# Kernel tuning notes

Hardware: AMD Instinct MI355X
Metric: run time of the kernel (lower is better)

The kernel has to match this reference:

```python
import jax, jax.numpy as jnp
import numpy as np

E = 8            # moe_num_experts
HIDDEN = 1024    # hidden_size
FFN = 4096       # ffn_hidden_size
TOKENS = 8192    # total tokens, pre-sorted by expert; balanced -> TOKENS // E per expert


def setup_inputs() -> dict:
    key = jax.random.key(0)
    k1, k2, k3 = jax.random.split(key, 3)
    x = jax.random.normal(k1, (TOKENS, HIDDEN), dtype=jnp.float32)
    # w1, w2 stored flattened as [E*FFN, HIDDEN], matching create_dmoe_expert_weights' view([-1, columns])
    w1 = jax.random.normal(k2, (E * FFN, HIDDEN), dtype=jnp.float32) * (1.0 / np.sqrt(HIDDEN))
    w2 = jax.random.normal(k3, (E * FFN, HIDDEN), dtype=jnp.float32) * (1.0 / np.sqrt(FFN))
    return {"x": x, "w1": w1, "w2": w2, "num_experts": E}


def reference(x, w1, w2, num_experts):
    # Block-diagonal topology of dMoE SparseMLP: tokens sorted by expert, each
    # expert owns a contiguous FFN slice of w1/w2. Equivalent grouped GEMM:
    #   out_e = gelu(x_e @ w1_e^T) @ w2_e   (megablocks gelu = tanh-approx GELU)
    tokens, hidden = x.shape
    ffn = w1.shape[0] // num_experts
    tpe = tokens // num_experts  # tokens per expert (balanced topology)
    xe = x.reshape(num_experts, tpe, hidden)        # [E, T/E, H]
    w1e = w1.reshape(num_experts, ffn, hidden)      # [E, F, H]
    w2e = w2.reshape(num_experts, ffn, hidden)      # [E, F, H]
    h = jax.nn.gelu(jnp.einsum('eth,efh->etf', xe, w1e), approximate=True)  # sdd + gelu
    out = jnp.einsum('etf,efh->eth', h, w2e)        # dsd
    return out.reshape(tokens, hidden)
```

## Files before the change

### kernel.cpp

```cpp
#include <hip/hip_runtime.h>
#include <hip/hip_bf16.h>
#include <stdint.h>

#define NE 8
#define HID 1024
#define FFN 4096
#define TOK 8192
#define TPE (TOK / NE)

typedef __attribute__((ext_vector_type(8))) short    bf16x8;
typedef __attribute__((ext_vector_type(4))) float    f32x4;
typedef __attribute__((ext_vector_type(4))) unsigned short ushort4v;
typedef __attribute__((ext_vector_type(8))) unsigned short ushort8v;


__device__ __forceinline__ unsigned short f2bf(float f) {
    union { float f; unsigned u; } c; c.f = f;
    unsigned r = c.u + 0x7fffu + ((c.u >> 16) & 1u);
    return (unsigned short)(r >> 16);
}

__device__ __forceinline__ float gelu_tanh(float x) {
    const float c0 = 0.7978845608028654f;
    const float c1 = 0.044715f;
    float u = c0 * (x + c1 * x * x * x);
    float t = 1.0f - 2.0f / (1.0f + __expf(2.0f * u));
    return 0.5f * x * (1.0f + t);
}

typedef const __attribute__((address_space(1))) void gbl_void_t;
typedef __attribute__((address_space(3))) void lds_void_t;

__device__ __forceinline__ void gload_lds16(const void* g, void* l) {
    __builtin_amdgcn_global_load_lds((gbl_void_t*)g, (lds_void_t*)l, 16, 0, 0);
}


__global__ void transpose_cvt(const float* __restrict__ in,
                              unsigned short* __restrict__ out) {
    __shared__ unsigned short tile[64][65];
    const int e  = blockIdx.z;
    const int f0 = blockIdx.x * 64;
    const int h0 = blockIdx.y * 64;
    const float*     src = in  + (size_t)e * FFN * HID;
    unsigned short*  dst = out + (size_t)e * HID * FFN;
    const int t  = threadIdx.x;
    const int tr = t >> 4;
    const int tc = (t & 15) * 4;
#pragma unroll
    for (int i = 0; i < 4; i++) {
        int f = i * 16 + tr;
        f32x4 v = *(const f32x4*)(src + (size_t)(f0 + f) * HID + h0 + tc);
#pragma unroll
        for (int j = 0; j < 4; j++) tile[f][tc + j] = f2bf(v[j]);
    }
    __syncthreads();
#pragma unroll
    for (int i = 0; i < 4; i++) {
        int h = i * 16 + tr;
        ushort4v o;
#pragma unroll
        for (int j = 0; j < 4; j++) o[j] = tile[tc + j][h];
        *(ushort4v*)(dst + (size_t)(h0 + h) * FFN + f0 + tc) = o;
    }
}


template <int GX, int GY>
__global__ __launch_bounds__(512, 2)
void gemm8f(const float* __restrict__ Af,
            const float* __restrict__ Bf,
            unsigned short* __restrict__ Cout, int M, int N, int K) {
    constexpr int BM = 256, BN = 256, BK = 64;
    constexpr int NH = 2, NI = 4, S = 32;
    constexpr int ABYTES = BM * BK * 2;
    constexpr int BBYTES = BN * BK * 2;
    constexpr int BUF = ABYTES + BBYTES;
    constexpr int NWG = NE * GX * GY;

    __shared__ __align__(16) char lds[2 * BUF];

    const int lin = blockIdx.x;
    const int wid = (lin & 7) * (NWG >> 3) + (lin >> 3);
    const int e   = wid / (GX * GY);
    const int rem = wid % (GX * GY);
    const int m0  = (rem % GX) * BM;
    const int n0  = (rem / GX) * BN;

    const float* Ae = Af + (size_t)e * M * K;
    const float* Be = Bf + (size_t)e * N * K;

    const int tid  = threadIdx.x;
    const int lane = tid & 63;
    const int w    = tid >> 6;
    const int wr   = w >> 2, wc = w & 3;
    const int fr   = lane & 15, fq = lane >> 4;

    const int rA  = tid >> 3;
    const int kb  = (tid & 7) * 16;
    const int kbs = kb ^ ((rA & 7) << 4);
    const int eoff = kbs >> 1;
    const float* aFb = Ae + (size_t)(m0 + rA) * K + eoff;
    const int   fB   = (rA / S) * 2 * S + (rA % S);
    const float* bFb = Be + (size_t)(n0 + fB) * K + eoff;
    char* dA0 = lds + rA * 128 + kb;
    char* dA1 = dA0 + BUF;
    char* dB0 = lds + ABYTES + fB * 128 + kb;
    char* dB1 = dB0 + BUF;

    auto LD_A = [&](int au, int kt, f32x4 (&g)[4]) {
        const float* s = aFb + (size_t)kt * 64;
        g[0] = *(const f32x4*)(s + (size_t)(au * 64) * K);
        g[1] = *(const f32x4*)(s + (size_t)(au * 64) * K + 4);
        g[2] = *(const f32x4*)(s + (size_t)(au * 64 + 128) * K);
        g[3] = *(const f32x4*)(s + (size_t)(au * 64 + 128) * K + 4);
    };
    auto LD_B = [&](int bu, int kt, f32x4 (&g)[4]) {
        const float* s = bFb + (size_t)kt * 64;
        g[0] = *(const f32x4*)(s + (size_t)(bu * S) * K);
        g[1] = *(const f32x4*)(s + (size_t)(bu * S) * K + 4);
        g[2] = *(const f32x4*)(s + (size_t)(bu * S + 128) * K);
        g[3] = *(const f32x4*)(s + (size_t)(bu * S + 128) * K + 4);
    };
    auto PACK = [&](const f32x4& lo, const f32x4& hi) {
        ushort8v o;
#pragma unroll
        for (int j = 0; j < 4; j++) { o[j] = f2bf(lo[j]); o[4 + j] = f2bf(hi[j]); }
        return o;
    };
    auto WR_A = [&](int au, char* d, f32x4 (&g)[4]) {
        *(ushort8v*)(d + (au * 64) * 128)       = PACK(g[0], g[1]);
        *(ushort8v*)(d + (au * 64 + 128) * 128) = PACK(g[2], g[3]);
    };
    auto WR_B = [&](int bu, char* d, f32x4 (&g)[4]) {
        *(ushort8v*)(d + (bu * S) * 128)        = PACK(g[0], g[1]);
        *(ushort8v*)(d + (bu * S + 128) * 128)  = PACK(g[2], g[3]);
    };

    const int kx0 = (fq * 16) ^ ((lane & 7) << 4);
    const char* paA = lds + (wr * 128 + fr) * 128;
    const char* paB = lds + ABYTES + (wc * (BN / 4) + fr) * 128;
    const char* pa0k0 = paA + kx0;        const char* pa0k1 = paA + (kx0 ^ 64);
    const char* pa1k0 = pa0k0 + BUF;      const char* pa1k1 = pa0k1 + BUF;
    const char* pb0k0 = paB + kx0;        const char* pb0k1 = paB + (kx0 ^ 64);
    const char* pb1k0 = pb0k0 + BUF;      const char* pb1k1 = pb0k1 + BUF;

    bf16x8 a[4][2], b0[NH][2], b1[NH][2];

    auto LDA = [&](const char* p0, const char* p1, int mq) {
#pragma unroll
        for (int mi = 0; mi < 4; mi++) {
            a[mi][0] = *(const bf16x8*)(p0 + mq * 8192 + mi * 2048);
            a[mi][1] = *(const bf16x8*)(p1 + mq * 8192 + mi * 2048);
        }
    };
    auto LDB = [&](const char* p0, const char* p1, int nq, bf16x8 (&bb)[NH][2]) {
#pragma unroll
        for (int ni = 0; ni < NH; ni++) {
            bb[ni][0] = *(const bf16x8*)(p0 + (nq * (BN / 8) + ni * 16) * 128);
            bb[ni][1] = *(const bf16x8*)(p1 + (nq * (BN / 8) + ni * 16) * 128);
        }
    };

    f32x4 acc[8][NI];

    auto MMQ = [&](int mq, int nq, bf16x8 (&bb)[NH][2]) {
        __builtin_amdgcn_s_setprio(1);
#pragma unroll
        for (int mi = 0; mi < 4; mi++)
#pragma unroll
            for (int ni = 0; ni < NH; ni++) {
                f32x4& c = acc[mq * 4 + mi][nq * NH + ni];
                c = __builtin_amdgcn_mfma_f32_16x16x32_bf16(a[mi][0], bb[ni][0], c, 0, 0, 0);
                c = __builtin_amdgcn_mfma_f32_16x16x32_bf16(a[mi][1], bb[ni][1], c, 0, 0, 0);
            }
        __builtin_amdgcn_s_setprio(0);
    };

#define MIDBAR()  __builtin_amdgcn_s_barrier();                                      \
                  asm volatile("s_waitcnt lgkmcnt(0)" ::: "memory")
#define ENDBAR()  __builtin_amdgcn_s_barrier()
#define LGHINT()  asm volatile("s_waitcnt lgkmcnt(8)" ::: "memory")

    const int NT   = K / BK;
    const int NTm1 = NT - 1;

    f32x4 gO[4], gE[4];
    {
        f32x4 t0[4];
        LD_A(0, 0, t0); WR_A(0, dA0, t0);
        LD_A(1, 0, t0); WR_A(1, dA0, t0);
        LD_B(0, 0, t0); WR_B(0, dB0, t0);
        LD_B(1, 0, t0); WR_B(1, dB0, t0);
        LD_A(0, 1, t0); WR_A(0, dA1, t0);
        LD_B(0, 1, t0); WR_B(0, dB1, t0);
        LD_B(1, 1, t0); WR_B(1, dB1, t0);
    }
    LD_A(1, 1, gO);
    LD_A(0, (2 < NT ? 2 : NTm1), gE);
#pragma unroll
    for (int i = 0; i < 8; i++)
#pragma unroll
        for (int j = 0; j < NI; j++) acc[i][j] = f32x4{0.f, 0.f, 0.f, 0.f};
    asm volatile("s_waitcnt lgkmcnt(0)" ::: "memory");
    __builtin_amdgcn_s_barrier();

    const int NW = NT / 2;
    for (int ww = 0; ww < NW; ++ww) {
        const int T = 2 * ww;
        const int kt2 = (T + 2 < NT) ? T + 2 : NTm1;
        const int kt3 = (T + 3 < NT) ? T + 3 : NTm1;
        const int kt4 = (T + 4 < NT) ? T + 4 : NTm1;

        LDA(pa0k0, pa0k1, 0); LDB(pb0k0, pb0k1, 0, b0); LGHINT();
        MIDBAR();
        WR_A(1, dA1, gO); LD_B(0, kt2, gO);
        MMQ(0, 0, b0); ENDBAR();
        LDB(pb0k0, pb0k1, 1, b1);
        MIDBAR();
        WR_A(0, dA0, gE); LD_B(1, kt2, gE);
        MMQ(0, 1, b1); ENDBAR();
        LDA(pa0k0, pa0k1, 1);
        MIDBAR();
        WR_B(0, dB0, gO); LD_A(1, kt2, gO);
        MMQ(1, 1, b1); ENDBAR();
        MIDBAR();
        WR_B(1, dB0, gE); LD_A(0, kt3, gE);
        MMQ(1, 0, b0); ENDBAR();
        LDA(pa1k0, pa1k1, 0); LDB(pb1k0, pb1k1, 0, b0); LGHINT();
        MIDBAR();
        WR_A(1, dA0, gO); LD_B(0, kt3, gO);
        MMQ(0, 0, b0); ENDBAR();
        LDB(pb1k0, pb1k1, 1, b1);
        MIDBAR();
        WR_A(0, dA1, gE); LD_B(1, kt3, gE);
        MMQ(0, 1, b1); ENDBAR();
        LDA(pa1k0, pa1k1, 1);
        MIDBAR();
        WR_B(0, dB1, gO); LD_A(1, kt3, gO);
        MMQ(1, 1, b1); ENDBAR();
        MIDBAR();
        WR_B(1, dB1, gE); LD_A(0, kt4, gE);
        MMQ(1, 0, b0); ENDBAR();
    }

    const int r0 = m0 + wr * 128 + fq * 4;
    const int c0 = n0 + wc * (BN / 4) + fr;
    unsigned short* C = Cout + (size_t)e * M * N;
#pragma unroll
    for (int mi = 0; mi < 8; mi++)
#pragma unroll
        for (int ni = 0; ni < NI; ni++) {
            int row = r0 + mi * 16, col = c0 + ni * 16;
#pragma unroll
            for (int r = 0; r < 4; r++)
                C[(size_t)(row + r) * N + col] = f2bf(gelu_tanh(acc[mi][ni][r]));
        }
#undef MIDBAR
#undef ENDBAR
#undef LGHINT
}


template <int BN, int GX, int GY, bool GELU>
__global__ __launch_bounds__(512, 2)
void gemm8p(const unsigned short* __restrict__ A,
            const unsigned short* __restrict__ B,
            void* __restrict__ Cout, int M, int N, int K) {
    constexpr int BM = 256, BK = 64;
    constexpr int NH = BN / 128;
    constexpr int NI = 2 * NH;
    constexpr int LB = BN / 128;
    constexpr int S  = BN / 8;
    constexpr int ABYTES = BM * BK * 2;
    constexpr int BBYTES = BN * BK * 2;
    constexpr int BUF = ABYTES + BBYTES;
    constexpr int VMC = 2 + 2 * LB;
    constexpr int NWG = NE * GX * GY;

    __shared__ __align__(16) char lds[2 * BUF];

    const int lin = blockIdx.x;
    const int wid = (lin & 7) * (NWG >> 3) + (lin >> 3);
    const int e   = wid / (GX * GY);
    const int rem = wid % (GX * GY);
    const int m0  = (rem % GX) * BM;
    const int n0  = (rem / GX) * BN;

    const size_t K2 = (size_t)K * 2;
    const char* Ae = (const char*)(A + (size_t)e * M * K);
    const char* Be = (const char*)(B + (size_t)e * N * K);

    const int tid  = threadIdx.x;
    const int lane = tid & 63;
    const int w    = tid >> 6;
    const int wr   = w >> 2, wc = w & 3;
    const int fr   = lane & 15, fq = lane >> 4;

    const int rA  = tid >> 3;
    const int kb  = (tid & 7) * 16;
    const int kbs = kb ^ ((rA & 7) << 4);
    const char* aptr = Ae + (size_t)(m0 + rA) * K2 + kbs;
    const int   fB   = (rA / S) * 2 * S + (rA % S);
    const char* bptr = Be + (size_t)(n0 + fB) * K2 + kbs;
    char* dA0 = lds + rA * 128 + kb;
    char* dA1 = dA0 + BUF;
    char* dB0 = lds + ABYTES + fB * 128 + kb;
    char* dB1 = dB0 + BUF;

    auto SA = [&](int au, int kt, char* d) {
        const char* s = aptr + (size_t)kt * 128;
#pragma unroll
        for (int i = 0; i < 2; i++)
            gload_lds16(s + (size_t)(au * 64 + i * 128) * K2,
                        d + (au * 64 + i * 128) * 128);
    };
    auto SB = [&](int bu, int kt, char* d) {
        const char* s = bptr + (size_t)kt * 128;
#pragma unroll
        for (int i = 0; i < LB; i++)
            gload_lds16(s + (size_t)(bu * S + i * 128) * K2,
                        d + (bu * S + i * 128) * 128);
    };

    const int kx0 = (fq * 16) ^ ((lane & 7) << 4);
    const char* paA = lds + (wr * 128 + fr) * 128;
    const char* paB = lds + ABYTES + (wc * (BN / 4) + fr) * 128;
    const char* pa0k0 = paA + kx0;        const char* pa0k1 = paA + (kx0 ^ 64);
    const char* pa1k0 = pa0k0 + BUF;      const char* pa1k1 = pa0k1 + BUF;
    const char* pb0k0 = paB + kx0;        const char* pb0k1 = paB + (kx0 ^ 64);
    const char* pb1k0 = pb0k0 + BUF;      const char* pb1k1 = pb0k1 + BUF;

    f32x4 acc[8][NI];
#pragma unroll
    for (int i = 0; i < 8; i++)
#pragma unroll
        for (int j = 0; j < NI; j++) acc[i][j] = f32x4{0.f, 0.f, 0.f, 0.f};

    bf16x8 a[4][2], b0[NH][2], b1[NH][2];

    auto LDA = [&](const char* p0, const char* p1, int mq) {
#pragma unroll
        for (int mi = 0; mi < 4; mi++) {
            a[mi][0] = *(const bf16x8*)(p0 + mq * 8192 + mi * 2048);
            a[mi][1] = *(const bf16x8*)(p1 + mq * 8192 + mi * 2048);
        }
    };
    auto LDB = [&](const char* p0, const char* p1, int nq, bf16x8 (&bb)[NH][2]) {
#pragma unroll
        for (int ni = 0; ni < NH; ni++) {
            bb[ni][0] = *(const bf16x8*)(p0 + (nq * (BN / 8) + ni * 16) * 128);
            bb[ni][1] = *(const bf16x8*)(p1 + (nq * (BN / 8) + ni * 16) * 128);
        }
    };
    auto MMQ = [&](int mq, int nq, bf16x8 (&bb)[NH][2]) {
        __builtin_amdgcn_s_setprio(1);
#pragma unroll
        for (int mi = 0; mi < 4; mi++)
#pragma unroll
            for (int ni = 0; ni < NH; ni++) {
                f32x4& c = acc[mq * 4 + mi][nq * NH + ni];
                c = __builtin_amdgcn_mfma_f32_16x16x32_bf16(a[mi][0], bb[ni][0], c, 0, 0, 0);
                c = __builtin_amdgcn_mfma_f32_16x16x32_bf16(a[mi][1], bb[ni][1], c, 0, 0, 0);
            }
        __builtin_amdgcn_s_setprio(0);
    };

#define MIDBAR()  __builtin_amdgcn_s_barrier();                                      \
                  asm volatile("s_waitcnt lgkmcnt(0)" ::: "memory")
#define ENDBAR()  __builtin_amdgcn_s_barrier()
#define LGHINT()  asm volatile("s_waitcnt lgkmcnt(8)" ::: "memory")
#define VMW()     asm volatile("s_waitcnt vmcnt(%0)" :: "n"(VMC) : "memory")

    const int NT   = K / BK;
    const int NTm1 = NT - 1;

    SA(0, 0, dA0); SB(0, 0, dB0); SB(1, 0, dB0); SA(1, 0, dA0);
    SA(0, 1, dA1); SB(0, 1, dB1); SB(1, 1, dB1);
    VMW();
    __builtin_amdgcn_s_barrier();

    const int NW = NT / 2;
    for (int ww = 0; ww < NW; ++ww) {
        const int T = 2 * ww;
        const int kt1 = T + 1;
        const int kt2 = (T + 2 < NT) ? T + 2 : NTm1;
        const int kt3 = (T + 3 < NT) ? T + 3 : NTm1;

        LDA(pa0k0, pa0k1, 0); LDB(pb0k0, pb0k1, 0, b0); SA(1, kt1, dA1); LGHINT();
        MIDBAR(); MMQ(0, 0, b0); ENDBAR();
        LDB(pb0k0, pb0k1, 1, b1); SA(0, kt2, dA0);
        MIDBAR(); MMQ(0, 1, b1); ENDBAR();
        LDA(pa0k0, pa0k1, 1); SB(0, kt2, dB0);
        MIDBAR(); MMQ(1, 1, b1); ENDBAR();
        SB(1, kt2, dB0);
        MIDBAR(); MMQ(1, 0, b0); VMW(); ENDBAR();
        LDA(pa1k0, pa1k1, 0); LDB(pb1k0, pb1k1, 0, b0); SA(1, kt2, dA0); LGHINT();
        MIDBAR(); MMQ(0, 0, b0); ENDBAR();
        LDB(pb1k0, pb1k1, 1, b1); SA(0, kt3, dA1);
        MIDBAR(); MMQ(0, 1, b1); ENDBAR();
        LDA(pa1k0, pa1k1, 1); SB(0, kt3, dB1);
        MIDBAR(); MMQ(1, 1, b1); ENDBAR();
        SB(1, kt3, dB1);
        MIDBAR(); MMQ(1, 0, b0); VMW(); ENDBAR();
    }
    asm volatile("s_waitcnt vmcnt(0)" ::: "memory");

    const int r0 = m0 + wr * 128 + fq * 4;
    const int c0 = n0 + wc * (BN / 4) + fr;
    if constexpr (GELU) {
        unsigned short* C = (unsigned short*)Cout + (size_t)e * M * N;
#pragma unroll
        for (int mi = 0; mi < 8; mi++)
#pragma unroll
            for (int ni = 0; ni < NI; ni++) {
                int row = r0 + mi * 16, col = c0 + ni * 16;
#pragma unroll
                for (int r = 0; r < 4; r++)
                    C[(size_t)(row + r) * N + col] = f2bf(gelu_tanh(acc[mi][ni][r]));
            }
    } else {
        float* C = (float*)Cout + (size_t)e * M * N;
#pragma unroll
        for (int mi = 0; mi < 8; mi++)
#pragma unroll
            for (int ni = 0; ni < NI; ni++) {
                int row = r0 + mi * 16, col = c0 + ni * 16;
#pragma unroll
                for (int r = 0; r < 4; r++)
                    C[(size_t)(row + r) * N + col] = acc[mi][ni][r];
            }
    }
#undef MIDBAR
#undef ENDBAR
#undef LGHINT
#undef VMW
}


__global__ void fused_fallback(const float* __restrict__ x,
                               const float* __restrict__ w1,
                               const float* __restrict__ w2,
                               float* __restrict__ out) {
    __shared__ float xs[HID];
    __shared__ float hs[FFN];
    const int tok = blockIdx.x;
    const int e   = tok / TPE;
    const float* w1e = w1 + (size_t)e * FFN * HID;
    const float* w2e = w2 + (size_t)e * FFN * HID;
    const int t = threadIdx.x;
    for (int i = t; i < HID; i += 256) xs[i] = x[(size_t)tok * HID + i];
    __syncthreads();
    for (int f = t; f < FFN; f += 256) {
        const float* wr_ = w1e + (size_t)f * HID;
        float s = 0.f;
        for (int k = 0; k < HID; k++) s += xs[k] * wr_[k];
        hs[f] = gelu_tanh(s);
    }
    __syncthreads();
    for (int h = t; h < HID; h += 256) {
        float s = 0.f;
        for (int f = 0; f < FFN; f++) s += hs[f] * w2e[(size_t)f * HID + h];
        out[(size_t)tok * HID + h] = s;
    }
}


extern "C" void kernel_launch(void* const* d_in, const int* in_sizes, int n_in,
                              void* d_out, int out_size, void* d_ws, size_t ws_size,
                              hipStream_t stream) {
    const float* x  = (const float*)d_in[0];
    const float* w1 = (const float*)d_in[1];
    const float* w2 = (const float*)d_in[2];
    float* out = (float*)d_out;

    const size_t W2B = (size_t)NE * FFN * HID * 2;
    const size_t HB  = (size_t)TOK * FFN * 2;
    const size_t need = W2B + HB;

    if (ws_size >= need) {
        char* ws = (char*)d_ws;
        unsigned short* w2t = (unsigned short*)ws;
        unsigned short* hb  = (unsigned short*)(ws + W2B);

        transpose_cvt<<<dim3(FFN / 64, HID / 64, NE), 256, 0, stream>>>(w2, w2t);

        gemm8f<TPE / 256, FFN / 256><<<NE * (TPE / 256) * (FFN / 256), 512, 0, stream>>>(
            x, w1, hb, TPE, FFN, HID);
        gemm8p<128, TPE / 256, HID / 128, false><<<NE * (TPE / 256) * (HID / 128), 512, 0, stream>>>(
            hb, w2t, out, TPE, HID, FFN);
    } else {
        fused_fallback<<<TOK, 256, 0, stream>>>(x, w1, w2, out);
    }
}
```

Before: 233.0 us.

## Remap second GEMM waves to a 4x2 grid with 64x64 per-wave tiles

The second grouped GEMM (h @ w2) drops its generic BN template and uses a fixed 256x128 block tile. The 8 waves are now arranged 4x2 instead of 2x4, so each wave computes a 64x64 sub-tile (interleaved rows and columns) rather than 128x32. This changes per-wave LDS read volume and register accumulator count, and is meant to improve operand reuse and reduce register pressure. The lgkmcnt hint wait is removed, which leaves the LDS load scheduling to the barriers.

Result: no change. 229.8 us (-1.4%).

```diff
diff --git a/kernel.cpp b/kernel.cpp
--- a/kernel.cpp
+++ b/kernel.cpp
@@ -262,20 +262,17 @@
 }
 
 
-template <int BN, int GX, int GY, bool GELU>
+template <int GX, int GY>
 __global__ __launch_bounds__(512, 2)
-void gemm8p(const unsigned short* __restrict__ A,
+void gemm2q(const unsigned short* __restrict__ A,
             const unsigned short* __restrict__ B,
-            void* __restrict__ Cout, int M, int N, int K) {
-    constexpr int BM = 256, BK = 64;
-    constexpr int NH = BN / 128;
-    constexpr int NI = 2 * NH;
-    constexpr int LB = BN / 128;
+            float* __restrict__ Cout, int M, int N, int K) {
+    constexpr int BM = 256, BN = 128, BK = 64;
     constexpr int S  = BN / 8;
     constexpr int ABYTES = BM * BK * 2;
     constexpr int BBYTES = BN * BK * 2;
     constexpr int BUF = ABYTES + BBYTES;
-    constexpr int VMC = 2 + 2 * LB;
+    constexpr int VMC = 4;
     constexpr int NWG = NE * GX * GY;
 
     __shared__ __align__(16) char lds[2 * BUF];
@@ -294,7 +291,8 @@
     const int tid  = threadIdx.x;
     const int lane = tid & 63;
     const int w    = tid >> 6;
-    const int wr   = w >> 2, wc = w & 3;
+    const int wr   = w >> 1;
+    const int wc   = w & 1;
     const int fr   = lane & 15, fq = lane >> 4;
 
     const int rA  = tid >> 3;
@@ -317,49 +315,48 @@
     };
     auto SB = [&](int bu, int kt, char* d) {
         const char* s = bptr + (size_t)kt * 128;
-#pragma unroll
-        for (int i = 0; i < LB; i++)
-            gload_lds16(s + (size_t)(bu * S + i * 128) * K2,
-                        d + (bu * S + i * 128) * 128);
-    };
-
-    const int kx0 = (fq * 16) ^ ((lane & 7) << 4);
-    const char* paA = lds + (wr * 128 + fr) * 128;
-    const char* paB = lds + ABYTES + (wc * (BN / 4) + fr) * 128;
+        gload_lds16(s + (size_t)(bu * S) * K2, d + (bu * S) * 128);
+    };
+
+    const int kx0   = (fq * 16) ^ ((lane & 7) << 4);
+    const int aBase = (wr & 1) * 32 + (wr >> 1) * 128;
+    const int bBase = wc * 64;
+    const char* paA = lds + (aBase + fr) * 128;
+    const char* paB = lds + ABYTES + (bBase + fr) * 128;
     const char* pa0k0 = paA + kx0;        const char* pa0k1 = paA + (kx0 ^ 64);
     const char* pa1k0 = pa0k0 + BUF;      const char* pa1k1 = pa0k1 + BUF;
     const char* pb0k0 = paB + kx0;        const char* pb0k1 = paB + (kx0 ^ 64);
     const char* pb1k0 = pb0k0 + BUF;      const char* pb1k1 = pb0k1 + BUF;
 
-    f32x4 acc[8][NI];
-#pragma unroll
-    for (int i = 0; i < 8; i++)
-#pragma unroll
-        for (int j = 0; j < NI; j++) acc[i][j] = f32x4{0.f, 0.f, 0.f, 0.f};
-
-    bf16x8 a[4][2], b0[NH][2], b1[NH][2];
+    f32x4 acc[4][4];
+#pragma unroll
+    for (int i = 0; i < 4; i++)
+#pragma unroll
+        for (int j = 0; j < 4; j++) acc[i][j] = f32x4{0.f, 0.f, 0.f, 0.f};
+
+    bf16x8 a[2][2], b0[2][2], b1[2][2];
 
     auto LDA = [&](const char* p0, const char* p1, int mq) {
 #pragma unroll
-        for (int mi = 0; mi < 4; mi++) {
+        for (int mi = 0; mi < 2; mi++) {
             a[mi][0] = *(const bf16x8*)(p0 + mq * 8192 + mi * 2048);
             a[mi][1] = *(const bf16x8*)(p1 + mq * 8192 + mi * 2048);
         }
     };
-    auto LDB = [&](const char* p0, const char* p1, int nq, bf16x8 (&bb)[NH][2]) {
-#pragma unroll
-        for (int ni = 0; ni < NH; ni++) {
-            bb[ni][0] = *(const bf16x8*)(p0 + (nq * (BN / 8) + ni * 16) * 128);
-            bb[ni][1] = *(const bf16x8*)(p1 + (nq * (BN / 8) + ni * 16) * 128);
-        }
-    };
-    auto MMQ = [&](int mq, int nq, bf16x8 (&bb)[NH][2]) {
+    auto LDB = [&](const char* p0, const char* p1, int nq, bf16x8 (&bb)[2][2]) {
+#pragma unroll
+        for (int ni = 0; ni < 2; ni++) {
+            bb[ni][0] = *(const bf16x8*)(p0 + (nq * 16 + ni * 32) * 128);
+            bb[ni][1] = *(const bf16x8*)(p1 + (nq * 16 + ni * 32) * 128);
+        }
+    };
+    auto MMQ = [&](int mq, int nq, bf16x8 (&bb)[2][2]) {
         __builtin_amdgcn_s_setprio(1);
 #pragma unroll
-        for (int mi = 0; mi < 4; mi++)
-#pragma unroll
-            for (int ni = 0; ni < NH; ni++) {
-                f32x4& c = acc[mq * 4 + mi][nq * NH + ni];
+        for (int mi = 0; mi < 2; mi++)
+#pragma unroll
+            for (int ni = 0; ni < 2; ni++) {
+                f32x4& c = acc[mq * 2 + mi][nq * 2 + ni];
                 c = __builtin_amdgcn_mfma_f32_16x16x32_bf16(a[mi][0], bb[ni][0], c, 0, 0, 0);
                 c = __builtin_amdgcn_mfma_f32_16x16x32_bf16(a[mi][1], bb[ni][1], c, 0, 0, 0);
             }
@@ -369,7 +366,6 @@
 #define MIDBAR()  __builtin_amdgcn_s_barrier();                                      \
                   asm volatile("s_waitcnt lgkmcnt(0)" ::: "memory")
 #define ENDBAR()  __builtin_amdgcn_s_barrier()
-#define LGHINT()  asm volatile("s_waitcnt lgkmcnt(8)" ::: "memory")
 #define VMW()     asm volatile("s_waitcnt vmcnt(%0)" :: "n"(VMC) : "memory")
 
     const int NT   = K / BK;
@@ -387,7 +383,7 @@
         const int kt2 = (T + 2 < NT) ? T + 2 : NTm1;
         const int kt3 = (T + 3 < NT) ? T + 3 : NTm1;
 
-        LDA(pa0k0, pa0k1, 0); LDB(pb0k0, pb0k1, 0, b0); SA(1, kt1, dA1); LGHINT();
+        LDA(pa0k0, pa0k1, 0); LDB(pb0k0, pb0k1, 0, b0); SA(1, kt1, dA1);
         MIDBAR(); MMQ(0, 0, b0); ENDBAR();
         LDB(pb0k0, pb0k1, 1, b1); SA(0, kt2, dA0);
         MIDBAR(); MMQ(0, 1, b1); ENDBAR();
@@ -395,7 +391,7 @@
         MIDBAR(); MMQ(1, 1, b1); ENDBAR();
         SB(1, kt2, dB0);
         MIDBAR(); MMQ(1, 0, b0); VMW(); ENDBAR();
-        LDA(pa1k0, pa1k1, 0); LDB(pb1k0, pb1k1, 0, b0); SA(1, kt2, dA0); LGHINT();
+        LDA(pa1k0, pa1k1, 0); LDB(pb1k0, pb1k1, 0, b0); SA(1, kt2, dA0);
         MIDBAR(); MMQ(0, 0, b0); ENDBAR();
         LDB(pb1k0, pb1k1, 1, b1); SA(0, kt3, dA1);
         MIDBAR(); MMQ(0, 1, b1); ENDBAR();
@@ -406,34 +402,21 @@
     }
     asm volatile("s_waitcnt vmcnt(0)" ::: "memory");
 
-    const int r0 = m0 + wr * 128 + fq * 4;
-    const int c0 = n0 + wc * (BN / 4) + fr;
-    if constexpr (GELU) {
-        unsigned short* C = (unsigned short*)Cout + (size_t)e * M * N;
-#pragma unroll
-        for (int mi = 0; mi < 8; mi++)
-#pragma unroll
-            for (int ni = 0; ni < NI; ni++) {
-                int row = r0 + mi * 16, col = c0 + ni * 16;
-#pragma unroll
-                for (int r = 0; r < 4; r++)
-                    C[(size_t)(row + r) * N + col] = f2bf(gelu_tanh(acc[mi][ni][r]));
-            }
-    } else {
-        float* C = (float*)Cout + (size_t)e * M * N;
-#pragma unroll
-        for (int mi = 0; mi < 8; mi++)
-#pragma unroll
-            for (int ni = 0; ni < NI; ni++) {
-                int row = r0 + mi * 16, col = c0 + ni * 16;
-#pragma unroll
-                for (int r = 0; r < 4; r++)
-                    C[(size_t)(row + r) * N + col] = acc[mi][ni][r];
-            }
-    }
+    const int r0 = m0 + aBase + fq * 4;
+    const int c0 = n0 + bBase + fr;
+    float* C = Cout + (size_t)e * M * N;
+#pragma unroll
+    for (int ai = 0; ai < 4; ai++)
+#pragma unroll
+        for (int aj = 0; aj < 4; aj++) {
+            int row = r0 + (ai >> 1) * 64 + (ai & 1) * 16;
+            int col = c0 + (aj >> 1) * 16 + (aj & 1) * 32;
+#pragma unroll
+            for (int r = 0; r < 4; r++)
+                C[(size_t)(row + r) * N + col] = acc[ai][aj][r];
+        }
 #undef MIDBAR
 #undef ENDBAR
-#undef LGHINT
 #undef VMW
 }
 
@@ -487,7 +470,7 @@
 
         gemm8f<TPE / 256, FFN / 256><<<NE * (TPE / 256) * (FFN / 256), 512, 0, stream>>>(
             x, w1, hb, TPE, FFN, HID);
-        gemm8p<128, TPE / 256, HID / 128, false><<<NE * (TPE / 256) * (HID / 128), 512, 0, stream>>>(
+        gemm2q<TPE / 256, HID / 128><<<NE * (TPE / 256) * (HID / 128), 512, 0, stream>>>(
             hb, w2t, out, TPE, HID, FFN);
     } else {
         fused_fallback<<<TOK, 256, 0, stream>>>(x, w1, w2, out);
```
